# Kernel optimization log

Measured on AMD Instinct MI355X. Metric: run time of the kernel, lower is better.

## Reference

```python
import jax, jax.numpy as jnp
import numpy as np

B, D, N = 128, 2, 8192
C_CENT, K, R = 32, 32, 0.25
BOTTLE = 8
BN_EPS = 1e-5


def setup_inputs() -> dict:
    key = jax.random.key(0)
    ks = jax.random.split(key, 12)
    w = lambda k, s: jax.random.normal(k, s, dtype=jnp.float32) * 0.05
    z = lambda s: jnp.zeros(s, jnp.float32)
    o = lambda s: jnp.ones(s, jnp.float32)
    return {
        "x": jax.random.normal(ks[0], (B, D, N), dtype=jnp.float32),
        "eps": jax.random.normal(ks[1], (B, BOTTLE), dtype=jnp.float32),
        "sa_c1_w": w(ks[2], (64, D)), "sa_c1_b": z((64,)),
        "sa_bn1_g": o((64,)), "sa_bn1_b": z((64,)),
        "sa_c2_w": w(ks[3], (128, 64)), "sa_c2_b": z((128,)),
        "sa_bn2_g": o((128,)), "sa_bn2_b": z((128,)),
        "sa_c3_w": w(ks[4], (256, 128)), "sa_c3_b": z((256,)),
        "sa_bn3_g": o((256,)), "sa_bn3_b": z((256,)),
        "sa_fc1_w": w(ks[5], (1024, 256 * C_CENT)), "sa_fc1_b": z((1024,)),
        "sa_bn4_g": o((1024,)), "sa_bn4_b": z((1024,)),
        "sa_fc2_w": w(ks[6], (256, 1024)), "sa_fc2_b": z((256,)),
        "sa_bn5_g": o((256,)), "sa_bn5_b": z((256,)),
        "sa_fc3_w": w(ks[7], (BOTTLE, 256)), "sa_fc3_b": z((BOTTLE,)),
        "fce1_w": w(ks[8], (BOTTLE, BOTTLE)), "fce1_b": z((BOTTLE,)),
        "fce2_w": w(ks[9], (BOTTLE, BOTTLE)), "fce2_b": z((BOTTLE,)),
        "dfc1_w": w(ks[10], (32, BOTTLE)), "dfc1_b": z((32,)),
        "dfc2_w": w(ks[11], (128, 32)), "dfc2_b": z((128,)),
        "dfc3_w": w(jax.random.fold_in(key, 99), (512, 128)), "dfc3_b": z((512,)),
    }


def _bn2d(x, g, b):
    m = jnp.mean(x, axis=(0, 2, 3), keepdims=True)
    v = jnp.var(x, axis=(0, 2, 3), keepdims=True)
    return (x - m) * jax.lax.rsqrt(v + BN_EPS) * g[None, :, None, None] + b[None, :, None, None]


def _bn1d(x, g, b):
    m = jnp.mean(x, axis=0, keepdims=True)
    v = jnp.var(x, axis=0, keepdims=True)
    return (x - m) * jax.lax.rsqrt(v + BN_EPS) * g[None, :] + b[None, :]


def _fps(points, n_centroids):
    # points: [B, D, N]; deterministic start at index 0 (torch uses randint)
    c0 = points[:, :, 0]                                   # [B, D]
    dist0 = jnp.sum((c0[:, :, None] - points) ** 2, axis=1)  # [B, N]

    def step(dist, _):
        ind = jnp.argmax(dist, axis=1)                      # [B]
        c = jnp.take_along_axis(points, ind[:, None, None], axis=2)[:, :, 0]  # [B, D]
        dist = jnp.minimum(dist, jnp.sum((c[:, :, None] - points) ** 2, axis=1))
        return dist, c

    _, cs = jax.lax.scan(step, dist0, None, length=n_centroids - 1)  # [C-1, B, D]
    cents = jnp.concatenate([c0[None], cs], axis=0)          # [C, B, D]
    return jnp.transpose(cents, (1, 2, 0))                   # [B, D, C]


def _group_points(points):
    b, _, n = points.shape
    cents = _fps(points, C_CENT)                             # [B, D, C]
    # squared pairwise distances centroid->point: [B, C, N]
    sq = (-2.0 * jnp.einsum('bdc,bdn->bcn', cents, points)
          + jnp.sum(cents ** 2, axis=1)[:, :, None]
          + jnp.sum(points ** 2, axis=1)[:, None, :])
    idx = jnp.broadcast_to(jnp.arange(n, dtype=jnp.int32), (b, C_CENT, n))
    idx = jnp.where(sq > R * R, jnp.int32(n), idx)
    idx = jnp.sort(idx, axis=-1)[:, :, :K]                   # [B, C, K]
    first = idx[:, :, :1]
    idx = jnp.where(idx == n, first, idx)
    bidx = jnp.arange(b)[:, None, None]
    grouped = points[bidx, :, idx]                            # [B, C, K, D]
    return jnp.transpose(grouped, (0, 3, 1, 2))               # [B, D, C, K]


def reference(x, eps, sa_c1_w, sa_c1_b, sa_bn1_g, sa_bn1_b, sa_c2_w, sa_c2_b,
              sa_bn2_g, sa_bn2_b, sa_c3_w, sa_c3_b, sa_bn3_g, sa_bn3_b,
              sa_fc1_w, sa_fc1_b, sa_bn4_g, sa_bn4_b, sa_fc2_w, sa_fc2_b,
              sa_bn5_g, sa_bn5_b, sa_fc3_w, sa_fc3_b, fce1_w, fce1_b,
              fce2_w, fce2_b, dfc1_w, dfc1_b, dfc2_w, dfc2_b, dfc3_w, dfc3_b):
    b = x.shape[0]
    g = _group_points(x)                                     # [B, D, C, K]
    h = jax.nn.relu(_bn2d(jnp.einsum('bdck,od->bock', g, sa_c1_w) + sa_c1_b[None, :, None, None], sa_bn1_g, sa_bn1_b))
    h = jax.nn.relu(_bn2d(jnp.einsum('bdck,od->bock', h, sa_c2_w) + sa_c2_b[None, :, None, None], sa_bn2_g, sa_bn2_b))
    h = jax.nn.relu(_bn2d(jnp.einsum('bdck,od->bock', h, sa_c3_w) + sa_c3_b[None, :, None, None], sa_bn3_g, sa_bn3_b))
    h = jnp.max(h, axis=3)                                   # [B, 256, C]
    h = h.reshape(b, 256 * C_CENT)
    h = jax.nn.relu(_bn1d(h @ sa_fc1_w.T + sa_fc1_b, sa_bn4_g, sa_bn4_b))
    h = jax.nn.relu(_bn1d(h @ sa_fc2_w.T + sa_fc2_b, sa_bn5_g, sa_bn5_b))
    feat = jax.nn.relu(h @ sa_fc3_w.T + sa_fc3_b)            # [B, 8]
    mu = feat @ fce1_w.T + fce1_b
    logvar = feat @ fce2_w.T + fce2_b
    zlat = eps * jnp.exp(0.5 * logvar) + mu                  # reparametrize
    d = jax.nn.relu(zlat @ dfc1_w.T + dfc1_b)
    d = jax.nn.relu(d @ dfc2_w.T + dfc2_b)
    d = d @ dfc3_w.T + dfc3_b
    out = d.reshape(-1, 2, 256)
    return out, mu, logvar
```

## Files before the change

kernel.cpp:

```cpp
#include <hip/hip_runtime.h>
#include <cstdint>
#include <cstddef>

#define NB   128
#define NPT  8192
#define NC   32
#define NK   32
#define MSP  131072
#define R2   0.0625f

typedef unsigned short u16;
typedef unsigned long long u64;
typedef __attribute__((ext_vector_type(8))) short short8v;
typedef __attribute__((ext_vector_type(4))) float f32x4;

static constexpr size_t OFF_CENTS  = 0;
static constexpr size_t OFF_GX     = 8192;
static constexpr size_t OFF_GY     = OFF_GX + 131072;
static constexpr size_t OFF_H1Q    = OFF_GY + 131072;
static constexpr size_t OFF_H2Q    = OFF_H1Q + 4194304;
static constexpr size_t OFF_MAXPRE = OFF_H1Q;
static constexpr size_t OFF_P3S    = OFF_H1Q + 1048576;
static constexpr size_t OFF_P3Q    = OFF_H1Q + 2097152;
static constexpr size_t OFF_PART1  = OFF_H2Q;
static constexpr size_t OFF_PART2  = OFF_H2Q + 4194304;
static constexpr size_t OFF_FC1    = OFF_H2Q + 8388608;
static constexpr size_t OFF_FC2    = OFF_FC1 + 131072;
static constexpr size_t OFF_W2Q    = OFF_FC2 + 32768;
static constexpr size_t OFF_W3Q    = OFF_W2Q + 4096;
static constexpr size_t OFF_PMOM   = OFF_W3Q + 16384;
static constexpr size_t OFF_P2S    = OFF_PMOM + 20480;
static constexpr size_t OFF_P2Q    = OFF_P2S + 131072;
static constexpr size_t OFF_SC1    = OFF_P2Q + 131072;
static constexpr size_t OFF_SH1    = OFF_SC1 + 64;
static constexpr size_t OFF_SC2    = OFF_SH1 + 64;
static constexpr size_t OFF_SH2    = OFF_SC2 + 128;
static constexpr size_t OFF_SC3    = OFF_SH2 + 128;
static constexpr size_t OFF_SH3    = OFF_SC3 + 256;
static constexpr size_t OFF_SC4    = OFF_SH3 + 256;
static constexpr size_t OFF_SH4    = OFF_SC4 + 1024;
static constexpr size_t OFF_SC5    = OFF_SH4 + 1024;
static constexpr size_t OFF_SH5    = OFF_SC5 + 256;
static constexpr size_t OFF_SC3E   = OFF_SH5 + 256;
static constexpr size_t OFF_SH3E   = OFF_SC3E + 8192;

__device__ __forceinline__ u16 f2bf(float f) {
  uint32_t u = __float_as_uint(f);
  u += 0x7FFFu + ((u >> 16) & 1u);
  return (u16)(u >> 16);
}
__device__ __forceinline__ float bf2f(u16 h) {
  return __uint_as_float(((uint32_t)h) << 16);
}
__device__ __forceinline__ void gload16(const void* g, void* l) {
  __builtin_amdgcn_global_load_lds(
      (const __attribute__((address_space(1))) void*)g,
      (__attribute__((address_space(3))) void*)l, 16, 0, 0);
}

__global__ __launch_bounds__(512) void fps_kernel(const float* __restrict__ x,
                                                  float* __restrict__ cents) {
  const int b = blockIdx.x, t = threadIdx.x;
  const int lane = t & 63, wid = t >> 6;
  const float* xb = x + (size_t)b * 2 * NPT;
  float px[16], py[16], dst[16];
  __shared__ float lpx[NPT], lpy[NPT];
  __shared__ u64 slot[2][8];
  __shared__ float cxs[NC], cys[NC];
#pragma unroll
  for (int k = 0; k < 16; k++) {
    const int id = t + k * 512;
    px[k] = xb[id];
    py[k] = xb[NPT + id];
    lpx[id] = px[k];
    lpy[id] = py[k];
  }
  const float c0x = xb[0], c0y = xb[NPT];
  if (t == 0) { cxs[0] = c0x; cys[0] = c0y; }
  u64 best = 0;
#pragma unroll
  for (int k = 0; k < 16; k++) {
    const float dx = __fsub_rn(c0x, px[k]);
    const float dy = __fsub_rn(c0y, py[k]);
    dst[k] = __fadd_rn(__fmul_rn(dx, dx), __fmul_rn(dy, dy));
    const u64 pk = ((u64)__float_as_uint(dst[k]) << 32) | (uint32_t)~(uint32_t)(t + k * 512);
    if (pk > best) best = pk;
  }
  __syncthreads();
  for (int j = 1; j < NC; j++) {
#pragma unroll
    for (int off = 1; off < 64; off <<= 1) {
      const u64 o = __shfl_xor(best, off);
      if (o > best) best = o;
    }
    const int pb = j & 1;
    if (lane == 0) slot[pb][wid] = best;
    __syncthreads();
    u64 w = slot[pb][0];
#pragma unroll
    for (int s = 1; s < 8; s++) {
      const u64 o = slot[pb][s];
      if (o > w) w = o;
    }
    const int wi = (int)~(uint32_t)w;
    const float wx = lpx[wi], wy = lpy[wi];
    if (t == 0) { cxs[j] = wx; cys[j] = wy; }
    best = 0;
#pragma unroll
    for (int k = 0; k < 16; k++) {
      const float dx = __fsub_rn(wx, px[k]);
      const float dy = __fsub_rn(wy, py[k]);
      const float nd = __fadd_rn(__fmul_rn(dx, dx), __fmul_rn(dy, dy));
      dst[k] = fminf(dst[k], nd);
      const u64 pk = ((u64)__float_as_uint(dst[k]) << 32) | (uint32_t)~(uint32_t)(t + k * 512);
      if (pk > best) best = pk;
    }
  }
  __syncthreads();
  if (t < NC) {
    cents[(size_t)b * 64 + t]      = cxs[t];
    cents[(size_t)b * 64 + 32 + t] = cys[t];
  }
}

__global__ __launch_bounds__(512) void group_kernel(const float* __restrict__ x,
                                                    const float* __restrict__ cents,
                                                    float* __restrict__ gx,
                                                    float* __restrict__ gy,
                                                    float* __restrict__ pmom) {
  const int b  = blockIdx.x & 127;
  const int cg = blockIdx.x >> 7;
  const int t = threadIdx.x;
  const int lane = t & 63, wid = t >> 6;
  const float* px = x + (size_t)b * 2 * NPT;
  const float* py = px + NPT;
  const int p0 = t * 16;

  float lx[16], ly[16], sp[16];
#pragma unroll
  for (int k = 0; k < 16; k += 4) {
    const float4 vx = *(const float4*)(px + p0 + k);
    const float4 vy = *(const float4*)(py + p0 + k);
    lx[k] = vx.x; lx[k + 1] = vx.y; lx[k + 2] = vx.z; lx[k + 3] = vx.w;
    ly[k] = vy.x; ly[k + 1] = vy.y; ly[k + 2] = vy.z; ly[k + 3] = vy.w;
  }
#pragma unroll
  for (int k = 0; k < 16; k++)
    sp[k] = __fadd_rn(__fmul_rn(lx[k], lx[k]), __fmul_rn(ly[k], ly[k]));

  __shared__ int idxs[4][NK];
  __shared__ int wtot[4][8];
  uint32_t mask[4];
  int ebase[4];

#pragma unroll
  for (int c = 0; c < 4; c++) {
    const int cc = cg * 4 + c;
    const float cx = cents[(size_t)b * 64 + cc];
    const float cy = cents[(size_t)b * 64 + 32 + cc];
    const float sc = __fadd_rn(__fmul_rn(cx, cx), __fmul_rn(cy, cy));
    uint32_t m = 0;
#pragma unroll
    for (int k = 0; k < 16; k++) {
      const float dot = __fadd_rn(__fmul_rn(cx, lx[k]), __fmul_rn(cy, ly[k]));
      const float sq  = __fadd_rn(__fadd_rn(__fmul_rn(-2.0f, dot), sc), sp[k]);
      if (!(sq > R2)) m |= (1u << k);
    }
    mask[c] = m;
    const int cnt = (int)__popc(m);
    int pre = cnt;
#pragma unroll
    for (int off = 1; off < 64; off <<= 1) {
      const int o = __shfl_up(pre, off);
      if (lane >= off) pre += o;
    }
    ebase[c] = pre - cnt;
    if (lane == 63) wtot[c][wid] = pre;
  }
  __syncthreads();
#pragma unroll
  for (int c = 0; c < 4; c++) {
    int off = 0;
#pragma unroll
    for (int w = 0; w < 8; w++) off += (w < wid) ? wtot[c][w] : 0;
    int pos = ebase[c] + off;
    uint32_t m = mask[c];
    while (m && pos < NK) {
      const int k = __ffs(m) - 1;
      idxs[c][pos] = p0 + k;
      m &= m - 1;
      pos++;
    }
  }
  __syncthreads();
  if (wid < 4) {
    int tot = 0;
#pragma unroll
    for (int w = 0; w < 8; w++) tot += wtot[wid][w];
    if (lane >= tot && lane < NK) idxs[wid][lane] = idxs[wid][0];
  }
  __syncthreads();
  if (wid < 4) {
    const int bc = b * 32 + cg * 4 + wid;
    float gxv = 0.f, gyv = 0.f;
    if (lane < NK) {
      const int id = idxs[wid][lane];
      gxv = px[id];
      gyv = py[id];
      const size_t s = (size_t)bc * NK + lane;
      gx[s] = gxv;
      gy[s] = gyv;
    }
    float sx = gxv, sy = gyv;
    float sxx = gxv * gxv, syy = gyv * gyv, sxy = gxv * gyv;
#pragma unroll
    for (int off = 1; off < 64; off <<= 1) {
      sx  += __shfl_xor(sx, off);
      sy  += __shfl_xor(sy, off);
      sxx += __shfl_xor(sxx, off);
      syy += __shfl_xor(syy, off);
      sxy += __shfl_xor(sxy, off);
    }
    if (lane == 0) {
      pmom[0 * 4096 + bc] = sx;
      pmom[1 * 4096 + bc] = sy;
      pmom[2 * 4096 + bc] = sxx;
      pmom[3 * 4096 + bc] = syy;
      pmom[4 * 4096 + bc] = sxy;
    }
  }
}

__global__ __launch_bounds__(256) void bn1fin_kernel(const float* __restrict__ pmom,
                                                     const float* __restrict__ w,
                                                     const float* __restrict__ gamma,
                                                     const float* __restrict__ beta,
                                                     float* __restrict__ sc,
                                                     float* __restrict__ sh) {
  const int t = threadIdx.x, lane = t & 63, wid = t >> 6;
  __shared__ float rr[5][4];
  __shared__ float red[5];
#pragma unroll
  for (int m = 0; m < 5; m++) {
    float a = 0.f;
#pragma unroll
    for (int i = 0; i < 4; i++) {
      const float4 v = *(const float4*)(pmom + m * 4096 + (t + i * 256) * 4);
      a += v.x + v.y + v.z + v.w;
    }
#pragma unroll
    for (int off = 1; off < 64; off <<= 1) a += __shfl_xor(a, off);
    if (lane == 0) rr[m][wid] = a;
  }
  __syncthreads();
  if (t == 0) {
#pragma unroll
    for (int m = 0; m < 5; m++) red[m] = rr[m][0] + rr[m][1] + rr[m][2] + rr[m][3];
  }
  __syncthreads();
  if (t < 64) {
    const double invM = 1.0 / (double)MSP;
    const double mx = red[0] * invM, my = red[1] * invM;
    const double exx = red[2] * invM, eyy = red[3] * invM, exy = red[4] * invM;
    const double w0 = w[2 * t], w1 = w[2 * t + 1];
    const double mean = w0 * mx + w1 * my;
    double var = w0 * w0 * (exx - mx * mx) + 2.0 * w0 * w1 * (exy - mx * my)
               + w1 * w1 * (eyy - my * my);
    if (var < 0.0) var = 0.0;
    const double s = (double)gamma[t] / sqrt(var + 1e-5);
    sc[t] = (float)s;
    sh[t] = (float)((double)beta[t] - mean * s);
  }
}

__global__ __launch_bounds__(256) void wquant_kernel(const float* __restrict__ c2w,
                                                     const float* __restrict__ c3w,
                                                     u16* __restrict__ w2q,
                                                     u16* __restrict__ w3qf) {
  const int id = blockIdx.x * 256 + threadIdx.x;
  if (id < 2048) {
    const int e = id * 4;
    const float4 v = *(const float4*)(c2w + e);
    uint2 q;
    q.x = (uint32_t)f2bf(v.x) | ((uint32_t)f2bf(v.y) << 16);
    q.y = (uint32_t)f2bf(v.z) | ((uint32_t)f2bf(v.w) << 16);
    *(uint2*)(w2q + e) = q;
  } else if (id < 2048 + 4096) {
    const int id2 = id - 2048;
    const int oc = id2 >> 4, k8 = (id2 & 15) * 8;
    const float4 v0 = *(const float4*)(c3w + oc * 128 + k8);
    const float4 v1 = *(const float4*)(c3w + oc * 128 + k8 + 4);
    uint4 q;
    q.x = (uint32_t)f2bf(v0.x) | ((uint32_t)f2bf(v0.y) << 16);
    q.y = (uint32_t)f2bf(v0.z) | ((uint32_t)f2bf(v0.w) << 16);
    q.z = (uint32_t)f2bf(v1.x) | ((uint32_t)f2bf(v1.y) << 16);
    q.w = (uint32_t)f2bf(v1.z) | ((uint32_t)f2bf(v1.w) << 16);
    const int off = ((((oc >> 4) * 4 + (k8 >> 5)) * 4 + ((k8 & 31) >> 3)) * 16 + (oc & 15)) * 8;
    *(uint4*)(w3qf + off) = q;
  }
}

__global__ __launch_bounds__(256) void finalize_kernel(
    const float* __restrict__ psum, const float* __restrict__ psq,
    int P, float invM,
    const float* __restrict__ gamma, const float* __restrict__ beta,
    float* __restrict__ scale, float* __restrict__ shift,
    float* __restrict__ scexp, float* __restrict__ shexp, int expand) {
  const int c = blockIdx.x, t = threadIdx.x;
  float s = 0.f, q = 0.f;
  for (int p = t; p < P; p += 256) {
    s += psum[(size_t)c * P + p];
    q += psq[(size_t)c * P + p];
  }
#pragma unroll
  for (int off = 1; off < 64; off <<= 1) {
    s += __shfl_xor(s, off);
    q += __shfl_xor(q, off);
  }
  __shared__ float r1[4], r2[4], bc2[2];
  if ((t & 63) == 0) { r1[t >> 6] = s; r2[t >> 6] = q; }
  __syncthreads();
  if (t == 0) {
    s = r1[0] + r1[1] + r1[2] + r1[3];
    q = r2[0] + r2[1] + r2[2] + r2[3];
    const float m = s * invM;
    float v = fmaf(-m, m, q * invM);
    v = fmaxf(v, 0.f);
    const float sc = gamma[c] * (float)(1.0 / sqrt((double)v + 1e-5));
    const float sh = fmaf(-m, sc, beta[c]);
    scale[c] = sc;
    shift[c] = sh;
    bc2[0] = sc;
    bc2[1] = sh;
  }
  __syncthreads();
  if (t < expand) {
    scexp[c * expand + t] = bc2[0];
    shexp[c * expand + t] = bc2[1];
  }
}

__global__ __launch_bounds__(256) void bncol_kernel(
    const float* __restrict__ in, int rows, int cols,
    const float* __restrict__ gamma, const float* __restrict__ beta,
    float* __restrict__ scale, float* __restrict__ shift) {
  const int jl = threadIdx.x & 63;
  const int rg = threadIdx.x >> 6;
  const int j = blockIdx.x * 64 + jl;
  float s = 0.f, q = 0.f;
  for (int r = rg; r < rows; r += 4) {
    const float v = in[(size_t)r * cols + j];
    s += v;
    q = fmaf(v, v, q);
  }
  __shared__ float rs[4][64], rq[4][64];
  rs[rg][jl] = s;
  rq[rg][jl] = q;
  __syncthreads();
  if (rg == 0) {
    s = rs[0][jl] + rs[1][jl] + rs[2][jl] + rs[3][jl];
    q = rq[0][jl] + rq[1][jl] + rq[2][jl] + rq[3][jl];
    const float m = s / (float)rows;
    float var = q / (float)rows - m * m;
    var = fmaxf(var, 0.f);
    const float sc = gamma[j] * (float)(1.0 / sqrt((double)var + 1e-5));
    scale[j] = sc;
    shift[j] = fmaf(-m, sc, beta[j]);
  }
}

__global__ __launch_bounds__(512) void conv2fused_kernel(
    const float* __restrict__ gx, const float* __restrict__ gy,
    const float* __restrict__ w1,
    const float* __restrict__ sc1, const float* __restrict__ sh1,
    const u16* __restrict__ wq,
    u16* __restrict__ outq,
    float* __restrict__ psum, float* __restrict__ psq) {
  constexpr int K = 64, OCB = 128, BS = 128, OCT = 128;
  constexpr int RB = K * 2;
  constexpr int STAGE = (OCB + BS) * RB;
  constexpr int EPI = BS * OCB * 2 + 4 * OCB * 2 * 4;
  constexpr int SMEM = STAGE > EPI ? STAGE : EPI;
  __shared__ __align__(16) char smem[SMEM + 1024];
  char* Wl = smem;
  char* Bl = smem + OCB * RB;
  float* par = (float*)(smem + SMEM);
  const int t = threadIdx.x;
  const int lane = t & 63, wid = t >> 6;
  const int sblk = blockIdx.x;
  const int s_base = sblk * BS;

  if (t < 64) {
    par[t]       = w1[t * 2];
    par[64 + t]  = w1[t * 2 + 1];
    par[128 + t] = sc1[t];
    par[192 + t] = sh1[t];
  }
  __syncthreads();

  {
    constexpr int CH = OCB * RB / 16, PW = CH / 8, NI = PW / 64;
#pragma unroll
    for (int j = 0; j < NI; j++) {
      const int c = wid * PW + j * 64 + lane;
      const int b = c * 16;
      const int oc = b / RB;
      const int off = b & (RB - 1);
      gload16((const char*)wq + (size_t)oc * RB + (off ^ ((oc & 7) << 4)),
              Wl + (wid * PW + j * 64) * 16);
    }
  }
  {
    const int sl = t >> 2;
    const int cq = t & 3;
    const float xx = gx[s_base + sl], yy = gy[s_base + sl];
    uint32_t pk[8];
#pragma unroll
    for (int h = 0; h < 8; h++) {
      const int c = cq * 16 + 2 * h;
      float v0 = fmaf(par[c],     xx, par[64 + c]     * yy);
      float v1 = fmaf(par[c + 1], xx, par[64 + c + 1] * yy);
      v0 = fmaxf(fmaf(v0, par[128 + c],     par[192 + c]),     0.f);
      v1 = fmaxf(fmaf(v1, par[128 + c + 1], par[192 + c + 1]), 0.f);
      pk[h] = (uint32_t)f2bf(v0) | ((uint32_t)f2bf(v1) << 16);
    }
    *(uint4*)(Bl + sl * RB + ((cq * 32)      ^ ((sl & 7) << 4))) = *(uint4*)&pk[0];
    *(uint4*)(Bl + sl * RB + ((cq * 32 + 16) ^ ((sl & 7) << 4))) = *(uint4*)&pk[4];
  }
  __syncthreads();

  const int wr = wid >> 2, wc = wid & 3;
  const int l15 = lane & 15, l4 = lane >> 4;
  f32x4 acc[4][2];
#pragma unroll
  for (int fo = 0; fo < 4; fo++)
#pragma unroll
    for (int fs = 0; fs < 2; fs++)
#pragma unroll
      for (int q = 0; q < 4; q++) acc[fo][fs][q] = 0.f;

#pragma unroll
  for (int ks = 0; ks < K / 32; ks++) {
    short8v a[4], bv[2];
#pragma unroll
    for (int f = 0; f < 4; f++) {
      const int oc = wr * 64 + f * 16 + l15;
      a[f] = *(const short8v*)(Wl + oc * RB + ((ks * 64 + l4 * 16) ^ ((oc & 7) << 4)));
    }
#pragma unroll
    for (int f = 0; f < 2; f++) {
      const int sl = wc * 32 + f * 16 + l15;
      bv[f] = *(const short8v*)(Bl + sl * RB + ((ks * 64 + l4 * 16) ^ ((sl & 7) << 4)));
    }
#pragma unroll
    for (int fo = 0; fo < 4; fo++)
#pragma unroll
      for (int fs = 0; fs < 2; fs++)
        acc[fo][fs] = __builtin_amdgcn_mfma_f32_16x16x32_bf16(a[fo], bv[fs], acc[fo][fs], 0, 0, 0);
  }
  __syncthreads();

  char* Dl = smem;
  float* sred1 = (float*)(smem + BS * OCB * 2);
  float* sred2 = sred1 + 4 * OCB;

#pragma unroll
  for (int fo = 0; fo < 4; fo++)
#pragma unroll
    for (int r = 0; r < 4; r++) {
      float s1 = acc[fo][0][r] + acc[fo][1][r];
      float s2 = fmaf(acc[fo][0][r], acc[fo][0][r], acc[fo][1][r] * acc[fo][1][r]);
#pragma unroll
      for (int off = 1; off < 16; off <<= 1) {
        s1 += __shfl_xor(s1, off);
        s2 += __shfl_xor(s2, off);
      }
      if (l15 == 0) {
        const int ocl = wr * 64 + fo * 16 + l4 * 4 + r;
        sred1[wc * OCB + ocl] = s1;
        sred2[wc * OCB + ocl] = s2;
      }
    }

#pragma unroll
  for (int fo = 0; fo < 4; fo++)
#pragma unroll
    for (int fs = 0; fs < 2; fs++) {
      const int sl = wc * 32 + fs * 16 + l15;
      const int ocl = wr * 64 + fo * 16 + l4 * 4;
      uint2 q;
      q.x = (uint32_t)f2bf(acc[fo][fs][0]) | ((uint32_t)f2bf(acc[fo][fs][1]) << 16);
      q.y = (uint32_t)f2bf(acc[fo][fs][2]) | ((uint32_t)f2bf(acc[fo][fs][3]) << 16);
      *(uint2*)(Dl + sl * 256 + ((ocl * 2) ^ ((sl & 7) << 4))) = q;
    }
  __syncthreads();

  if (t < OCB) {
    psum[(size_t)t * 1024 + sblk] =
        sred1[t] + sred1[OCB + t] + sred1[2 * OCB + t] + sred1[3 * OCB + t];
    psq[(size_t)t * 1024 + sblk] =
        sred2[t] + sred2[OCB + t] + sred2[2 * OCB + t] + sred2[3 * OCB + t];
  }
#pragma unroll
  for (int i = 0; i < 4; i++) {
    const int c = t + i * 512;
    const int sl = c >> 4, slot = c & 15;
    const uint4 v = *(const uint4*)(Dl + sl * 256 + ((slot * 16) ^ ((sl & 7) << 4)));
    *(uint4*)(outq + (size_t)(s_base + sl) * OCT + slot * 8) = v;
  }
}

__global__ __launch_bounds__(512) void conv3_kernel(
    const u16* __restrict__ act,
    const u16* __restrict__ wqf,
    const float* __restrict__ ascale, const float* __restrict__ ashift,
    float* __restrict__ psum, float* __restrict__ psq,
    float* __restrict__ maxpre) {
  constexpr int K = 128, RB = 256;
  __shared__ __align__(16) char Bl[64 * RB];
  const int t = threadIdx.x;
  const int lane = t & 63, wid = t >> 6;
  const int ws = wid & 1, wo = wid >> 1;
  const int sblk = blockIdx.x;
  const int l15 = lane & 15, l4 = lane >> 4;
  const int s_base = sblk * 64;

  short8v b[4][4];
  {
    const int ocq0 = wo * 4;
#pragma unroll
    for (int fo = 0; fo < 4; fo++)
#pragma unroll
      for (int ks = 0; ks < 4; ks++)
        b[fo][ks] = *(const short8v*)(wqf + ((((ocq0 + fo) * 4 + ks) * 4 + l4) * 16 + l15) * 8);
  }

  {
    const int kk0 = (t & 15) * 8;
    const float4 scA = *(const float4*)(ascale + kk0);
    const float4 scB = *(const float4*)(ascale + kk0 + 4);
    const float4 shA = *(const float4*)(ashift + kk0);
    const float4 shB = *(const float4*)(ashift + kk0 + 4);
    const float scr[8] = {scA.x, scA.y, scA.z, scA.w, scB.x, scB.y, scB.z, scB.w};
    const float shr[8] = {shA.x, shA.y, shA.z, shA.w, shB.x, shB.y, shB.z, shB.w};
#pragma unroll
    for (int i = 0; i < 2; i++) {
      const int sl = (t >> 4) + i * 32;
      const uint4 raw = *(const uint4*)(act + (size_t)(s_base + sl) * K + kk0);
      const u16* rp = (const u16*)&raw;
      uint32_t pk[4];
#pragma unroll
      for (int h = 0; h < 4; h++) {
        const float f0 = fmaxf(fmaf(bf2f(rp[2 * h]),     scr[2 * h],     shr[2 * h]),     0.f);
        const float f1 = fmaxf(fmaf(bf2f(rp[2 * h + 1]), scr[2 * h + 1], shr[2 * h + 1]), 0.f);
        pk[h] = (uint32_t)f2bf(f0) | ((uint32_t)f2bf(f1) << 16);
      }
      *(uint4*)(Bl + sl * RB + ((kk0 * 2) ^ ((sl & 7) << 4))) = *(uint4*)pk;
    }
  }
  __syncthreads();

  f32x4 acc[2][4];
#pragma unroll
  for (int fs = 0; fs < 2; fs++)
#pragma unroll
    for (int fo = 0; fo < 4; fo++)
#pragma unroll
      for (int q = 0; q < 4; q++) acc[fs][fo][q] = 0.f;

#pragma unroll
  for (int ks = 0; ks < 4; ks++) {
    short8v a[2];
#pragma unroll
    for (int fs = 0; fs < 2; fs++) {
      const int srow = ws * 32 + fs * 16 + l15;
      a[fs] = *(const short8v*)(Bl + srow * RB + ((ks * 64 + l4 * 16) ^ ((srow & 7) << 4)));
    }
#pragma unroll
    for (int fs = 0; fs < 2; fs++)
#pragma unroll
      for (int fo = 0; fo < 4; fo++)
        acc[fs][fo] = __builtin_amdgcn_mfma_f32_16x16x32_bf16(a[fs], b[fo][ks], acc[fs][fo], 0, 0, 0);
  }

  const int gid = sblk * 2 + ws;
#pragma unroll
  for (int fo = 0; fo < 4; fo++) {
    float s1 = acc[0][fo][0], s2 = acc[0][fo][0] * acc[0][fo][0];
    float mx = acc[0][fo][0];
#pragma unroll
    for (int fs = 0; fs < 2; fs++)
#pragma unroll
      for (int r = 0; r < 4; r++) {
        if (fs == 0 && r == 0) continue;
        const float v = acc[fs][fo][r];
        s1 += v;
        s2 = fmaf(v, v, s2);
        mx = fmaxf(mx, v);
      }
    s1 += __shfl_xor(s1, 16); s1 += __shfl_xor(s1, 32);
    s2 += __shfl_xor(s2, 16); s2 += __shfl_xor(s2, 32);
    mx = fmaxf(mx, __shfl_xor(mx, 16));
    mx = fmaxf(mx, __shfl_xor(mx, 32));
    if (l4 == 0) {
      const int oc = wo * 64 + fo * 16 + l15;
      psum[(size_t)oc * 4096 + gid] = s1;
      psq [(size_t)oc * 4096 + gid] = s2;
      maxpre[(size_t)oc * 4096 + gid] = mx;
    }
  }
}

template <int KL, bool TRANS, bool GATHER>
__global__ __launch_bounds__(512) void fcmfma_kernel(
    const float* __restrict__ A,
    const float* __restrict__ W,
    const float* __restrict__ ascale, const float* __restrict__ ashift,
    float* __restrict__ part,
    int Ntot, int Ktot) {
  __shared__ __align__(16) char smem[65536];
  char* Wh = smem;
  char* Wl = smem + 16384;
  char* Ah = smem + 32768;
  char* Al = smem + 49152;
  const int t = threadIdx.x;
  const int lane = t & 63, wid = t >> 6;
  const int sblk = blockIdx.x;
  const int n_base = blockIdx.y * 128;
  const int k_begin = sblk * KL;
  const int kq = t & 15;
  const int r0 = t >> 4;
  const int kk = kq * 4;
  const int wn = wid & 1, wm = wid >> 1;
  const int l15 = lane & 15, l4 = lane >> 4;

  f32x4 acc[4][2];
#pragma unroll
  for (int fo = 0; fo < 4; fo++)
#pragma unroll
    for (int fs = 0; fs < 2; fs++)
#pragma unroll
      for (int q = 0; q < 4; q++) acc[fo][fs][q] = 0.f;

  float4 wv[4], av[4], tsc, tsh;
  {
    const int kabs = k_begin + kk;
    if constexpr (TRANS) {
      tsc = *(const float4*)(ascale + kabs);
      tsh = *(const float4*)(ashift + kabs);
    }
#pragma unroll
    for (int i = 0; i < 4; i++) {
      const int row = r0 + i * 32;
      wv[i] = *(const float4*)(W + (size_t)(n_base + row) * Ktot + kabs);
      if constexpr (GATHER)
        av[i] = *(const float4*)(A + (size_t)(kabs >> 5) * 4096 + row * 32 + (kabs & 31));
      else
        av[i] = *(const float4*)(A + (size_t)row * Ktot + kabs);
    }
  }

  for (int c0 = 0; c0 < KL; c0 += 64) {
#pragma unroll
    for (int i = 0; i < 4; i++) {
      const int row = r0 + i * 32;
      const int byte = row * 128 + ((kk * 2) ^ ((row & 7) << 4));
      {
        const float4 v = wv[i];
        const u16 h0 = f2bf(v.x), h1 = f2bf(v.y), h2 = f2bf(v.z), h3 = f2bf(v.w);
        uint2 hv, lv;
        hv.x = (uint32_t)h0 | ((uint32_t)h1 << 16);
        hv.y = (uint32_t)h2 | ((uint32_t)h3 << 16);
        lv.x = (uint32_t)f2bf(v.x - bf2f(h0)) | ((uint32_t)f2bf(v.y - bf2f(h1)) << 16);
        lv.y = (uint32_t)f2bf(v.z - bf2f(h2)) | ((uint32_t)f2bf(v.w - bf2f(h3)) << 16);
        *(uint2*)(Wh + byte) = hv;
        *(uint2*)(Wl + byte) = lv;
      }
      {
        float4 v = av[i];
        if constexpr (TRANS) {
          v.x = fmaxf(fmaf(v.x, tsc.x, tsh.x), 0.f);
          v.y = fmaxf(fmaf(v.y, tsc.y, tsh.y), 0.f);
          v.z = fmaxf(fmaf(v.z, tsc.z, tsh.z), 0.f);
          v.w = fmaxf(fmaf(v.w, tsc.w, tsh.w), 0.f);
        }
        const u16 h0 = f2bf(v.x), h1 = f2bf(v.y), h2 = f2bf(v.z), h3 = f2bf(v.w);
        uint2 hv, lv;
        hv.x = (uint32_t)h0 | ((uint32_t)h1 << 16);
        hv.y = (uint32_t)h2 | ((uint32_t)h3 << 16);
        lv.x = (uint32_t)f2bf(v.x - bf2f(h0)) | ((uint32_t)f2bf(v.y - bf2f(h1)) << 16);
        lv.y = (uint32_t)f2bf(v.z - bf2f(h2)) | ((uint32_t)f2bf(v.w - bf2f(h3)) << 16);
        *(uint2*)(Ah + byte) = hv;
        *(uint2*)(Al + byte) = lv;
      }
    }
    __syncthreads();
    if (c0 + 64 < KL) {
      const int kabs = k_begin + c0 + 64 + kk;
      if constexpr (TRANS) {
        tsc = *(const float4*)(ascale + kabs);
        tsh = *(const float4*)(ashift + kabs);
      }
#pragma unroll
      for (int i = 0; i < 4; i++) {
        const int row = r0 + i * 32;
        wv[i] = *(const float4*)(W + (size_t)(n_base + row) * Ktot + kabs);
        if constexpr (GATHER)
          av[i] = *(const float4*)(A + (size_t)(kabs >> 5) * 4096 + row * 32 + (kabs & 31));
        else
          av[i] = *(const float4*)(A + (size_t)row * Ktot + kabs);
      }
    }
#pragma unroll
    for (int ks = 0; ks < 2; ks++) {
      short8v ah[4], al_[4], bh[2], bl[2];
#pragma unroll
      for (int f = 0; f < 4; f++) {
        const int r = wn * 64 + f * 16 + l15;
        const int byte = r * 128 + ((ks * 64 + l4 * 16) ^ ((r & 7) << 4));
        ah[f]  = *(const short8v*)(Wh + byte);
        al_[f] = *(const short8v*)(Wl + byte);
      }
#pragma unroll
      for (int f = 0; f < 2; f++) {
        const int r = wm * 32 + f * 16 + l15;
        const int byte = r * 128 + ((ks * 64 + l4 * 16) ^ ((r & 7) << 4));
        bh[f] = *(const short8v*)(Ah + byte);
        bl[f] = *(const short8v*)(Al + byte);
      }
#pragma unroll
      for (int fo = 0; fo < 4; fo++)
#pragma unroll
        for (int fs = 0; fs < 2; fs++) {
          acc[fo][fs] = __builtin_amdgcn_mfma_f32_16x16x32_bf16(ah[fo],  bh[fs], acc[fo][fs], 0, 0, 0);
          acc[fo][fs] = __builtin_amdgcn_mfma_f32_16x16x32_bf16(ah[fo],  bl[fs], acc[fo][fs], 0, 0, 0);
          acc[fo][fs] = __builtin_amdgcn_mfma_f32_16x16x32_bf16(al_[fo], bh[fs], acc[fo][fs], 0, 0, 0);
        }
    }
    __syncthreads();
  }
#pragma unroll
  for (int fo = 0; fo < 4; fo++) {
    const int n0 = n_base + wn * 64 + fo * 16 + l4 * 4;
#pragma unroll
    for (int fs = 0; fs < 2; fs++) {
      const int m = wm * 32 + fs * 16 + l15;
      *(float4*)(part + ((size_t)sblk * 128 + m) * Ntot + n0) =
          make_float4(acc[fo][fs][0], acc[fo][fs][1], acc[fo][fs][2], acc[fo][fs][3]);
    }
  }
}

__global__ __launch_bounds__(256) void fcreduce_kernel(const float* __restrict__ part,
                                                       float* __restrict__ out,
                                                       int total, int S) {
  const int id = blockIdx.x * 256 + threadIdx.x;
  if (id >= total) return;
  float s = 0.f;
  for (int p = 0; p < S; p++) s += part[(size_t)p * total + id];
  out[id] = s;
}

__global__ __launch_bounds__(128) void tail_kernel(
    const float* __restrict__ fc2raw, const float* __restrict__ scale5, const float* __restrict__ shift5,
    const float* __restrict__ w3, const float* __restrict__ b3,
    const float* __restrict__ e1w, const float* __restrict__ e1b,
    const float* __restrict__ e2w, const float* __restrict__ e2b,
    const float* __restrict__ eps,
    const float* __restrict__ d1w, const float* __restrict__ d1b,
    const float* __restrict__ d2w, const float* __restrict__ d2b,
    const float* __restrict__ d3w, const float* __restrict__ d3b,
    float* __restrict__ out) {
  const int b = blockIdx.x, t = threadIdx.x;
  __shared__ float h5[256], feat[8], z[8], d1[32], d2[128];
  for (int i = t; i < 256; i += 128) {
    const float v = fc2raw[(size_t)b * 256 + i];
    h5[i] = fmaxf(fmaf(v, scale5[i], shift5[i]), 0.f);
  }
  __syncthreads();
  if (t < 64) {
    const int o = t >> 3, p = t & 7;
    const float* wr = w3 + o * 256 + p * 32;
    const float* hr = h5 + p * 32;
    float s = 0.f;
    for (int i = 0; i < 32; i++) s = fmaf(hr[i], wr[i], s);
    s += __shfl_xor(s, 1);
    s += __shfl_xor(s, 2);
    s += __shfl_xor(s, 4);
    if (p == 0) feat[o] = fmaxf(s + b3[o], 0.f);
  }
  __syncthreads();
  if (t < 8) {
    float mu = e1b[t], lv = e2b[t];
    for (int j = 0; j < 8; j++) {
      mu = fmaf(feat[j], e1w[t * 8 + j], mu);
      lv = fmaf(feat[j], e2w[t * 8 + j], lv);
    }
    out[65536 + b * 8 + t] = mu;
    out[66560 + b * 8 + t] = lv;
    z[t] = fmaf(eps[b * 8 + t], expf(0.5f * lv), mu);
  }
  __syncthreads();
  if (t < 32) {
    float s = d1b[t];
    for (int j = 0; j < 8; j++) s = fmaf(z[j], d1w[t * 8 + j], s);
    d1[t] = fmaxf(s, 0.f);
  }
  __syncthreads();
  {
    float s = d2b[t];
    for (int j = 0; j < 32; j++) s = fmaf(d1[j], d2w[t * 32 + j], s);
    d2[t] = fmaxf(s, 0.f);
  }
  __syncthreads();
  for (int o = t; o < 512; o += 128) {
    float s = d3b[o];
    for (int j = 0; j < 128; j++) s = fmaf(d2[j], d3w[o * 128 + j], s);
    out[(size_t)b * 512 + o] = s;
  }
}

extern "C" void kernel_launch(void* const* d_in, const int* in_sizes, int n_in,
                              void* d_out, int out_size, void* d_ws, size_t ws_size,
                              hipStream_t stream) {
  const float* x    = (const float*)d_in[0];
  const float* eps  = (const float*)d_in[1];
  const float* c1w  = (const float*)d_in[2];
  const float* bn1g = (const float*)d_in[4];
  const float* bn1b = (const float*)d_in[5];
  const float* c2w  = (const float*)d_in[6];
  const float* bn2g = (const float*)d_in[8];
  const float* bn2b = (const float*)d_in[9];
  const float* c3w  = (const float*)d_in[10];
  const float* bn3g = (const float*)d_in[12];
  const float* bn3b = (const float*)d_in[13];
  const float* f1w  = (const float*)d_in[14];
  const float* bn4g = (const float*)d_in[16];
  const float* bn4b = (const float*)d_in[17];
  const float* f2w  = (const float*)d_in[18];
  const float* bn5g = (const float*)d_in[20];
  const float* bn5b = (const float*)d_in[21];
  const float* f3w  = (const float*)d_in[22];
  const float* f3b  = (const float*)d_in[23];
  const float* e1w  = (const float*)d_in[24];
  const float* e1b  = (const float*)d_in[25];
  const float* e2w  = (const float*)d_in[26];
  const float* e2b  = (const float*)d_in[27];
  const float* d1w  = (const float*)d_in[28];
  const float* d1b  = (const float*)d_in[29];
  const float* d2w  = (const float*)d_in[30];
  const float* d2b  = (const float*)d_in[31];
  const float* d3w  = (const float*)d_in[32];
  const float* d3b  = (const float*)d_in[33];

  float* ws = (float*)d_ws;
  float* cents  = ws + OFF_CENTS;
  float* gx     = ws + OFF_GX;
  float* gy     = ws + OFF_GY;
  u16*   h2q    = (u16*)(ws + OFF_H2Q);
  u16*   w2q    = (u16*)(ws + OFF_W2Q);
  u16*   w3qf   = (u16*)(ws + OFF_W3Q);
  float* pmom   = ws + OFF_PMOM;
  float* maxpre = ws + OFF_MAXPRE;
  float* part1  = ws + OFF_PART1;
  float* part2  = ws + OFF_PART2;
  float* fc1o   = ws + OFF_FC1;
  float* fc2o   = ws + OFF_FC2;
  float* p2s = ws + OFF_P2S, *p2q = ws + OFF_P2Q;
  float* p3s = ws + OFF_P3S, *p3q = ws + OFF_P3Q;
  float* sc1 = ws + OFF_SC1, *sh1 = ws + OFF_SH1;
  float* sc2 = ws + OFF_SC2, *sh2 = ws + OFF_SH2;
  float* sc3 = ws + OFF_SC3, *sh3 = ws + OFF_SH3;
  float* sc4 = ws + OFF_SC4, *sh4 = ws + OFF_SH4;
  float* sc5 = ws + OFF_SC5, *sh5 = ws + OFF_SH5;
  float* sc3e = ws + OFF_SC3E, *sh3e = ws + OFF_SH3E;

  wquant_kernel<<<24, 256, 0, stream>>>(c2w, c3w, w2q, w3qf);
  fps_kernel<<<NB, 512, 0, stream>>>(x, cents);
  group_kernel<<<1024, 512, 0, stream>>>(x, cents, gx, gy, pmom);

  bn1fin_kernel<<<1, 256, 0, stream>>>(pmom, c1w, bn1g, bn1b, sc1, sh1);

  conv2fused_kernel<<<1024, 512, 0, stream>>>(gx, gy, c1w, sc1, sh1, w2q,
                                              h2q, p2s, p2q);
  finalize_kernel<<<128, 256, 0, stream>>>(p2s, p2q, 1024, 1.f / MSP, bn2g, bn2b,
                                           sc2, sh2, nullptr, nullptr, 0);

  conv3_kernel<<<2048, 512, 0, stream>>>(h2q, w3qf, sc2, sh2, p3s, p3q, maxpre);
  finalize_kernel<<<256, 256, 0, stream>>>(p3s, p3q, 4096, 1.f / MSP, bn3g, bn3b,
                                           sc3, sh3, sc3e, sh3e, 32);

  fcmfma_kernel<256, true, true><<<dim3(32, 8), 512, 0, stream>>>(
      maxpre, f1w, sc3e, sh3e, part1, 1024, 8192);
  fcreduce_kernel<<<512, 256, 0, stream>>>(part1, fc1o, 131072, 32);
  bncol_kernel<<<16, 256, 0, stream>>>(fc1o, 128, 1024, bn4g, bn4b, sc4, sh4);

  fcmfma_kernel<128, true, false><<<dim3(8, 2), 512, 0, stream>>>(
      fc1o, f2w, sc4, sh4, part2, 256, 1024);
  fcreduce_kernel<<<128, 256, 0, stream>>>(part2, fc2o, 32768, 8);
  bncol_kernel<<<4, 256, 0, stream>>>(fc2o, 128, 256, bn5g, bn5b, sc5, sh5);

  tail_kernel<<<NB, 128, 0, stream>>>(fc2o, sc5, sh5, f3w, f3b, e1w, e1b, e2w, e2b, eps,
                                      d1w, d1b, d2w, d2b, d3w, d3b, (float*)d_out);
}
```

Baseline: 194.1 us.

## Fold weight quantization into FPS, widen grouping blocks, fuse fc2 reduce with BN stats

Moves the bf16 weight-quantization work into the first 12 blocks of the FPS kernel and drops its separate launch. The grouping kernel now handles 8 centroids per block using all 8 waves, which halves its grid. The fc2 partial-sum reduction is merged with the BatchNorm column statistics into one kernel. Together these cut launch count and per-launch overhead in a chain of small kernels. In exchange, the quantization work lengthens a few FPS blocks, and the fused reduce runs on only 4 blocks.

```diff
diff --git a/kernel.cpp b/kernel.cpp
--- a/kernel.cpp
+++ b/kernel.cpp
@@ -59,9 +59,38 @@
 }
 
 __global__ __launch_bounds__(512) void fps_kernel(const float* __restrict__ x,
-                                                  float* __restrict__ cents) {
+                                                  float* __restrict__ cents,
+                                                  const float* __restrict__ c2w,
+                                                  const float* __restrict__ c3w,
+                                                  u16* __restrict__ w2q,
+                                                  u16* __restrict__ w3qf) {
   const int b = blockIdx.x, t = threadIdx.x;
   const int lane = t & 63, wid = t >> 6;
+
+  if (b < 12) {
+    const int id = b * 512 + t;
+    if (id < 2048) {
+      const int e = id * 4;
+      const float4 v = *(const float4*)(c2w + e);
+      uint2 q;
+      q.x = (uint32_t)f2bf(v.x) | ((uint32_t)f2bf(v.y) << 16);
+      q.y = (uint32_t)f2bf(v.z) | ((uint32_t)f2bf(v.w) << 16);
+      *(uint2*)(w2q + e) = q;
+    } else {
+      const int id2 = id - 2048;
+      const int oc = id2 >> 4, k8 = (id2 & 15) * 8;
+      const float4 v0 = *(const float4*)(c3w + oc * 128 + k8);
+      const float4 v1 = *(const float4*)(c3w + oc * 128 + k8 + 4);
+      uint4 q;
+      q.x = (uint32_t)f2bf(v0.x) | ((uint32_t)f2bf(v0.y) << 16);
+      q.y = (uint32_t)f2bf(v0.z) | ((uint32_t)f2bf(v0.w) << 16);
+      q.z = (uint32_t)f2bf(v1.x) | ((uint32_t)f2bf(v1.y) << 16);
+      q.w = (uint32_t)f2bf(v1.z) | ((uint32_t)f2bf(v1.w) << 16);
+      const int off = ((((oc >> 4) * 4 + (k8 >> 5)) * 4 + ((k8 & 31) >> 3)) * 16 + (oc & 15)) * 8;
+      *(uint4*)(w3qf + off) = q;
+    }
+  }
+
   const float* xb = x + (size_t)b * 2 * NPT;
   float px[16], py[16], dst[16];
   __shared__ float lpx[NPT], lpy[NPT];
@@ -148,14 +177,14 @@
   for (int k = 0; k < 16; k++)
     sp[k] = __fadd_rn(__fmul_rn(lx[k], lx[k]), __fmul_rn(ly[k], ly[k]));
 
-  __shared__ int idxs[4][NK];
-  __shared__ int wtot[4][8];
-  uint32_t mask[4];
-  int ebase[4];
-
-#pragma unroll
-  for (int c = 0; c < 4; c++) {
-    const int cc = cg * 4 + c;
+  __shared__ int idxs[8][NK];
+  __shared__ int wtot[8][8];
+  uint32_t mask[8];
+  int ebase[8];
+
+#pragma unroll
+  for (int c = 0; c < 8; c++) {
+    const int cc = cg * 8 + c;
     const float cx = cents[(size_t)b * 64 + cc];
     const float cy = cents[(size_t)b * 64 + 32 + cc];
     const float sc = __fadd_rn(__fmul_rn(cx, cx), __fmul_rn(cy, cy));
@@ -179,7 +208,7 @@
   }
   __syncthreads();
 #pragma unroll
-  for (int c = 0; c < 4; c++) {
+  for (int c = 0; c < 8; c++) {
     int off = 0;
 #pragma unroll
     for (int w = 0; w < 8; w++) off += (w < wid) ? wtot[c][w] : 0;
@@ -193,15 +222,15 @@
     }
   }
   __syncthreads();
-  if (wid < 4) {
+  {
     int tot = 0;
 #pragma unroll
     for (int w = 0; w < 8; w++) tot += wtot[wid][w];
     if (lane >= tot && lane < NK) idxs[wid][lane] = idxs[wid][0];
   }
   __syncthreads();
-  if (wid < 4) {
-    const int bc = b * 32 + cg * 4 + wid;
+  {
+    const int bc = b * 32 + cg * 8 + wid;
     float gxv = 0.f, gyv = 0.f;
     if (lane < NK) {
       const int id = idxs[wid][lane];
@@ -273,33 +302,6 @@
   }
 }
 
-__global__ __launch_bounds__(256) void wquant_kernel(const float* __restrict__ c2w,
-                                                     const float* __restrict__ c3w,
-                                                     u16* __restrict__ w2q,
-                                                     u16* __restrict__ w3qf) {
-  const int id = blockIdx.x * 256 + threadIdx.x;
-  if (id < 2048) {
-    const int e = id * 4;
-    const float4 v = *(const float4*)(c2w + e);
-    uint2 q;
-    q.x = (uint32_t)f2bf(v.x) | ((uint32_t)f2bf(v.y) << 16);
-    q.y = (uint32_t)f2bf(v.z) | ((uint32_t)f2bf(v.w) << 16);
-    *(uint2*)(w2q + e) = q;
-  } else if (id < 2048 + 4096) {
-    const int id2 = id - 2048;
-    const int oc = id2 >> 4, k8 = (id2 & 15) * 8;
-    const float4 v0 = *(const float4*)(c3w + oc * 128 + k8);
-    const float4 v1 = *(const float4*)(c3w + oc * 128 + k8 + 4);
-    uint4 q;
-    q.x = (uint32_t)f2bf(v0.x) | ((uint32_t)f2bf(v0.y) << 16);
-    q.y = (uint32_t)f2bf(v0.z) | ((uint32_t)f2bf(v0.w) << 16);
-    q.z = (uint32_t)f2bf(v1.x) | ((uint32_t)f2bf(v1.y) << 16);
-    q.w = (uint32_t)f2bf(v1.z) | ((uint32_t)f2bf(v1.w) << 16);
-    const int off = ((((oc >> 4) * 4 + (k8 >> 5)) * 4 + ((k8 & 31) >> 3)) * 16 + (oc & 15)) * 8;
-    *(uint4*)(w3qf + off) = q;
-  }
-}
-
 __global__ __launch_bounds__(256) void finalize_kernel(
     const float* __restrict__ psum, const float* __restrict__ psq,
     int P, float invM,
@@ -350,6 +352,39 @@
   float s = 0.f, q = 0.f;
   for (int r = rg; r < rows; r += 4) {
     const float v = in[(size_t)r * cols + j];
+    s += v;
+    q = fmaf(v, v, q);
+  }
+  __shared__ float rs[4][64], rq[4][64];
+  rs[rg][jl] = s;
+  rq[rg][jl] = q;
+  __syncthreads();
+  if (rg == 0) {
+    s = rs[0][jl] + rs[1][jl] + rs[2][jl] + rs[3][jl];
+    q = rq[0][jl] + rq[1][jl] + rq[2][jl] + rq[3][jl];
+    const float m = s / (float)rows;
+    float var = q / (float)rows - m * m;
+    var = fmaxf(var, 0.f);
+    const float sc = gamma[j] * (float)(1.0 / sqrt((double)var + 1e-5));
+    scale[j] = sc;
+    shift[j] = fmaf(-m, sc, beta[j]);
+  }
+}
+
+__global__ __launch_bounds__(256) void fcredcol_kernel(
+    const float* __restrict__ part, float* __restrict__ out,
+    const float* __restrict__ gamma, const float* __restrict__ beta,
+    float* __restrict__ scale, float* __restrict__ shift,
+    int S, int rows, int cols) {
+  const int jl = threadIdx.x & 63;
+  const int rg = threadIdx.x >> 6;
+  const int j = blockIdx.x * 64 + jl;
+  const int total = rows * cols;
+  float s = 0.f, q = 0.f;
+  for (int r = rg; r < rows; r += 4) {
+    float v = 0.f;
+    for (int p = 0; p < S; p++) v += part[(size_t)p * total + r * cols + j];
+    out[(size_t)r * cols + j] = v;
     s += v;
     q = fmaf(v, v, q);
   }
@@ -875,9 +910,8 @@
   float* sc5 = ws + OFF_SC5, *sh5 = ws + OFF_SH5;
   float* sc3e = ws + OFF_SC3E, *sh3e = ws + OFF_SH3E;
 
-  wquant_kernel<<<24, 256, 0, stream>>>(c2w, c3w, w2q, w3qf);
-  fps_kernel<<<NB, 512, 0, stream>>>(x, cents);
-  group_kernel<<<1024, 512, 0, stream>>>(x, cents, gx, gy, pmom);
+  fps_kernel<<<NB, 512, 0, stream>>>(x, cents, c2w, c3w, w2q, w3qf);
+  group_kernel<<<512, 512, 0, stream>>>(x, cents, gx, gy, pmom);
 
   bn1fin_kernel<<<1, 256, 0, stream>>>(pmom, c1w, bn1g, bn1b, sc1, sh1);
 
@@ -897,8 +931,8 @@
 
   fcmfma_kernel<128, true, false><<<dim3(8, 2), 512, 0, stream>>>(
       fc1o, f2w, sc4, sh4, part2, 256, 1024);
-  fcreduce_kernel<<<128, 256, 0, stream>>>(part2, fc2o, 32768, 8);
-  bncol_kernel<<<4, 256, 0, stream>>>(fc2o, 128, 256, bn5g, bn5b, sc5, sh5);
+  fcredcol_kernel<<<4, 256, 0, stream>>>(part2, fc2o, bn5g, bn5b, sc5, sh5,
+                                         8, 128, 256);
 
   tail_kernel<<<NB, 128, 0, stream>>>(fc2o, sc5, sh5, f3w, f3b, e1w, e1b, e2w, e2b, eps,
                                       d1w, d1b, d2w, d2b, d3w, d3b, (float*)d_out);
```

New measurement: 241.8 us. +24.6%, slower.
